# Optimization experiments

Hardware: AMD Instinct MI355X
Metric: run time of the kernel (lower is better)

Reference implementation:

```python
import jax, jax.numpy as jnp
import numpy as np

WINDOW_SIZE = 7
NB_HEADS = 8


def _relative_position_index(ws: int) -> np.ndarray:
    coords = np.stack(np.meshgrid(np.arange(ws), np.arange(ws), indexing='ij'))  # [2, ws, ws]
    flat = coords.reshape(2, -1)  # [2, ws*ws]
    rel = flat[:, :, None] - flat[:, None, :]  # [2, N, N]
    rel = rel.transpose(1, 2, 0)
    rel[:, :, 0] += ws - 1
    rel[:, :, 1] += ws - 1
    rel[:, :, 0] *= 2 * ws - 1
    return rel.sum(-1).astype(np.int64)  # [N, N]


def setup_inputs() -> dict:
    key = jax.random.key(0)
    ks = jax.random.split(key, 7)
    B_, N, C = 2048, WINDOW_SIZE * WINDOW_SIZE, 256
    nW = 64
    return {
        'x': jax.random.normal(ks[0], (B_, N, C), dtype=jnp.float32),
        'mask': jax.random.normal(ks[1], (nW, N, N), dtype=jnp.float32),
        'qkv_w': jax.random.normal(ks[2], (C, 3 * C), dtype=jnp.float32) * 0.02,
        'qkv_b': jax.random.normal(ks[3], (3 * C,), dtype=jnp.float32) * 0.02,
        'proj_w': jax.random.normal(ks[4], (C, C), dtype=jnp.float32) * 0.02,
        'proj_b': jax.random.normal(ks[5], (C,), dtype=jnp.float32) * 0.02,
        'bias_table': jax.random.normal(ks[6], ((2 * WINDOW_SIZE - 1) ** 2, NB_HEADS), dtype=jnp.float32) * 0.02,
    }


def reference(x, mask, qkv_w, qkv_b, proj_w, proj_b, bias_table):
    B_, N, C = x.shape
    h = NB_HEADS
    d = C // h
    rpi = jnp.asarray(_relative_position_index(WINDOW_SIZE))  # [N, N] int

    qkv = x @ qkv_w + qkv_b  # [B_, N, 3C]
    qkv = qkv.reshape(B_, N, 3, h, d).transpose(2, 0, 3, 1, 4)  # [3, B_, h, N, d]
    q, k, v = qkv[0], qkv[1], qkv[2]

    scale = d ** -0.5
    attn = jnp.einsum('bhnd,bhmd->bhnm', q * scale, k)  # [B_, h, N, N]

    # relative position bias gather: [N*N, h] -> [h, N, N]
    bias = bias_table[rpi.reshape(-1)].reshape(N, N, h).transpose(2, 0, 1)
    attn = attn + bias[None]

    nW = mask.shape[0]
    attn = attn.reshape(B_ // nW, nW, h, N, N) + mask[None, :, None]  # broadcast mask over heads
    attn = attn.reshape(B_, h, N, N)
    attn = jax.nn.softmax(attn, axis=-1)

    out = jnp.einsum('bhnm,bhmd->bhnd', attn, v)  # [B_, h, N, d]
    out = out.transpose(0, 2, 1, 3).reshape(B_, N, C)
    return out @ proj_w + proj_b
```

## Files before the change

kernel.cpp:

```cpp
#include <hip/hip_runtime.h>
#include <hip/hip_bf16.h>

typedef __attribute__((ext_vector_type(8))) short bf16x8;
typedef __attribute__((ext_vector_type(4))) float f32x4;

__device__ __forceinline__ void load_lds16(const void* g, void* l) {
    __builtin_amdgcn_global_load_lds(
        (const __attribute__((address_space(1))) unsigned int*)g,
        (__attribute__((address_space(3))) unsigned int*)l, 16, 0, 0);
}

__global__ void k_cvt_x(const float* __restrict__ x, __hip_bfloat16* __restrict__ xb, int n4) {
    for (int i = blockIdx.x * blockDim.x + threadIdx.x; i < n4; i += gridDim.x * blockDim.x) {
        float4 v = ((const float4*)x)[i];
        union { ushort4 u; __hip_bfloat16 h[4]; } o;
        o.h[0] = __float2bfloat16(v.x); o.h[1] = __float2bfloat16(v.y);
        o.h[2] = __float2bfloat16(v.z); o.h[3] = __float2bfloat16(v.w);
        ((ushort4*)xb)[i] = o.u;
    }
}

__global__ void k_prep_w(const float* __restrict__ qkv_w, const float* __restrict__ qkv_b,
                         const float* __restrict__ proj_w, const float* __restrict__ bias_table,
                         __hip_bfloat16* __restrict__ qwT, __hip_bfloat16* __restrict__ pwT,
                         float* __restrict__ qb_s, float* __restrict__ biasH) {
    const float scale = 0.17677669529663687f;
    int i = blockIdx.x * 256 + threadIdx.x;
    if (i < 768 * 256) {
        int nc = i >> 8, kc = i & 255;
        float v = qkv_w[kc * 768 + nc];
        if (nc < 256) v *= scale;
        qwT[i] = __float2bfloat16(v);
    } else if (i < 768 * 256 + 256 * 256) {
        int j = i - 768 * 256;
        int nc = j >> 8, kc = j & 255;
        pwT[j] = __float2bfloat16(proj_w[kc * 256 + nc]);
    } else if (i < 768 * 256 + 256 * 256 + 768) {
        int j = i - (768 * 256 + 256 * 256);
        qb_s[j] = qkv_b[j] * (j < 256 ? scale : 1.f);
    } else if (i < 768 * 256 + 256 * 256 + 768 + 8 * 2401) {
        int j = i - (768 * 256 + 256 * 256 + 768);
        int h = j / 2401, r = j % 2401;
        int n = r / 49, m = r % 49;
        int i1 = n / 7, j1 = n % 7, i2 = m / 7, j2 = m % 7;
        int rpi = (i1 - i2 + 6) * 13 + (j1 - j2 + 6);
        biasH[j] = bias_table[rpi * 8 + h];
    }
}

template <bool OUT_BF16>
__global__ __launch_bounds__(256, 2)
void gemm_bt(const __hip_bfloat16* __restrict__ A,
             const __hip_bfloat16* __restrict__ BT,
             const float* __restrict__ bias,
             void* __restrict__ Cout,
             int M, int N, int K) {
    __shared__ alignas(16) __hip_bfloat16 sA[2][128][64];
    __shared__ alignas(16) __hip_bfloat16 sB[2][128][64];
    const int bn = blockIdx.x, bm = blockIdx.y;
    const int tid = threadIdx.x, wid = tid >> 6, lane = tid & 63;
    const int g = lane >> 4, c0 = lane & 15;
    const int r8 = lane >> 3;
    const int sl = (lane & 7) ^ r8;
    const int wrow = (wid >> 1) * 64, wcol = (wid & 1) * 64;
    const __hip_bfloat16* Abase = A + (size_t)bm * 128 * K;
    const __hip_bfloat16* Bbase = BT + (size_t)bn * 128 * K;
    const int KT = K >> 6;

    f32x4 acc[4][4];
#pragma unroll
    for (int i = 0; i < 4; ++i)
#pragma unroll
        for (int j = 0; j < 4; ++j)
#pragma unroll
            for (int r = 0; r < 4; ++r) acc[i][j][r] = 0.f;

    auto stage = [&](int buf, int kt) {
        const __hip_bfloat16* Ak = Abase + kt * 64;
        const __hip_bfloat16* Bk = Bbase + kt * 64;
        char* la = (char*)&sA[buf][0][0];
        char* lb = (char*)&sB[buf][0][0];
#pragma unroll
        for (int i = 0; i < 4; ++i) {
            int chunk = wid * 4 + i;
            int row = chunk * 8 + r8;
            load_lds16(Ak + (size_t)row * K + sl * 8, la + chunk * 1024);
            load_lds16(Bk + (size_t)row * K + sl * 8, lb + chunk * 1024);
        }
    };

    stage(0, 0);
    __syncthreads();
    for (int kt = 0; kt < KT; ++kt) {
        int cur = kt & 1;
        if (kt + 1 < KT) stage(cur ^ 1, kt + 1);
        const char* la = (const char*)&sA[cur][0][0];
        const char* lb = (const char*)&sB[cur][0][0];
#pragma unroll
        for (int ks = 0; ks < 2; ++ks) {
            bf16x8 af[4], bfr[4];
            int sbyte = ((ks * 4 + g) ^ (c0 & 7)) * 16;
#pragma unroll
            for (int t = 0; t < 4; ++t) {
                int ra = wrow + t * 16 + c0;
                af[t] = *(const bf16x8*)(la + ra * 128 + sbyte);
                int rb = wcol + t * 16 + c0;
                bfr[t] = *(const bf16x8*)(lb + rb * 128 + sbyte);
            }
#pragma unroll
            for (int rt = 0; rt < 4; ++rt)
#pragma unroll
                for (int ct = 0; ct < 4; ++ct)
                    acc[rt][ct] = __builtin_amdgcn_mfma_f32_16x16x32_bf16(
                        af[rt], bfr[ct], acc[rt][ct], 0, 0, 0);
        }
        __syncthreads();
    }

    float bv[4];
#pragma unroll
    for (int ct = 0; ct < 4; ++ct) bv[ct] = bias[bn * 128 + wcol + ct * 16 + c0];
#pragma unroll
    for (int rt = 0; rt < 4; ++rt) {
#pragma unroll
        for (int ct = 0; ct < 4; ++ct) {
#pragma unroll
            for (int reg = 0; reg < 4; ++reg) {
                int row = bm * 128 + wrow + rt * 16 + g * 4 + reg;
                int col = bn * 128 + wcol + ct * 16 + c0;
                float v = acc[rt][ct][reg] + bv[ct];
                if (OUT_BF16)
                    ((__hip_bfloat16*)Cout)[(size_t)row * N + col] = __float2bfloat16(v);
                else
                    ((float*)Cout)[(size_t)row * N + col] = v;
            }
        }
    }
}

__global__ __launch_bounds__(64)
void attn_win(const __hip_bfloat16* __restrict__ qkv,
              const float* __restrict__ mask,
              const float* __restrict__ biasH,
              __hip_bfloat16* __restrict__ attout) {
    __shared__ alignas(16) __hip_bfloat16 vt[32][72];
    __shared__ alignas(16) __hip_bfloat16 pl[64][64];
    const int bh = blockIdx.x;
    const int b = bh >> 3, h = bh & 7;
    const int lane = threadIdx.x & 63, g = lane >> 4, c0 = lane & 15;
    const __hip_bfloat16* qb = qkv + (size_t)b * 49 * 768 + h * 32;

    for (int i = lane; i < 32 * 15; i += 64) {
        int c = i / 15, m = 49 + i % 15;
        vt[c][m] = __float2bfloat16(0.f);
    }
    for (int i = lane; i < 784; i += 64) {
        int m = i >> 4, c2 = (i & 15) * 2;
        ushort2 v = *(const ushort2*)(qb + (size_t)m * 768 + 512 + c2);
        *(unsigned short*)&vt[c2][m] = v.x;
        *(unsigned short*)&vt[c2 + 1][m] = v.y;
    }

    const bf16x8 z8 = {};
    bf16x8 kf[4];
#pragma unroll
    for (int ct = 0; ct < 4; ++ct) {
        int m = ct * 16 + c0;
        kf[ct] = (m < 49) ? *(const bf16x8*)(qb + (size_t)m * 768 + 256 + g * 8) : z8;
    }
    __syncthreads();

    const float* mrow = mask + (size_t)(b & 63) * 2401;
    const float* brow = biasH + (size_t)h * 2401;
    const f32x4 zf = {0.f, 0.f, 0.f, 0.f};

#pragma unroll
    for (int rt = 0; rt < 4; ++rt) {
        int nA = rt * 16 + c0;
        bf16x8 qf = (nA < 49) ? *(const bf16x8*)(qb + (size_t)nA * 768 + g * 8) : z8;
        f32x4 s[4];
#pragma unroll
        for (int ct = 0; ct < 4; ++ct)
            s[ct] = __builtin_amdgcn_mfma_f32_16x16x32_bf16(qf, kf[ct], zf, 0, 0, 0);
#pragma unroll
        for (int reg = 0; reg < 4; ++reg) {
            int n = rt * 16 + 4 * g + reg;
            int nc = n < 49 ? n : 48;
            const float* br = brow + nc * 49;
            const float* mr = mrow + nc * 49;
#pragma unroll
            for (int ct = 0; ct < 4; ++ct) {
                int m = ct * 16 + c0;
                float v = s[ct][reg];
                v = (m < 49) ? v + br[m] + mr[m] : -1e30f;
                s[ct][reg] = v;
            }
            float mx = fmaxf(fmaxf(s[0][reg], s[1][reg]), fmaxf(s[2][reg], s[3][reg]));
            mx = fmaxf(mx, __shfl_xor(mx, 1));
            mx = fmaxf(mx, __shfl_xor(mx, 2));
            mx = fmaxf(mx, __shfl_xor(mx, 4));
            mx = fmaxf(mx, __shfl_xor(mx, 8));
            float sum = 0.f;
#pragma unroll
            for (int ct = 0; ct < 4; ++ct) {
                float e = __expf(s[ct][reg] - mx);
                s[ct][reg] = e;
                sum += e;
            }
            sum += __shfl_xor(sum, 1);
            sum += __shfl_xor(sum, 2);
            sum += __shfl_xor(sum, 4);
            sum += __shfl_xor(sum, 8);
            float inv = 1.f / sum;
#pragma unroll
            for (int ct = 0; ct < 4; ++ct) {
                int m = ct * 16 + c0;
                int byte = (n * 128 + m * 2) ^ ((n & 7) << 4);
                *(__hip_bfloat16*)((char*)&pl[0][0] + byte) = __float2bfloat16(s[ct][reg] * inv);
            }
        }
    }
    __syncthreads();

    f32x4 o[4][2];
#pragma unroll
    for (int rt = 0; rt < 4; ++rt)
#pragma unroll
        for (int ci = 0; ci < 2; ++ci)
#pragma unroll
            for (int r = 0; r < 4; ++r) o[rt][ci][r] = 0.f;
#pragma unroll
    for (int kt = 0; kt < 2; ++kt) {
        bf16x8 pa[4], vb[2];
#pragma unroll
        for (int rt = 0; rt < 4; ++rt) {
            int row = rt * 16 + c0;
            int byte = row * 128 + (((kt * 4 + g) ^ (row & 7)) << 4);
            pa[rt] = *(const bf16x8*)((const char*)&pl[0][0] + byte);
        }
#pragma unroll
        for (int ci = 0; ci < 2; ++ci)
            vb[ci] = *(const bf16x8*)(&vt[ci * 16 + c0][kt * 32 + g * 8]);
#pragma unroll
        for (int rt = 0; rt < 4; ++rt)
#pragma unroll
            for (int ci = 0; ci < 2; ++ci)
                o[rt][ci] = __builtin_amdgcn_mfma_f32_16x16x32_bf16(pa[rt], vb[ci], o[rt][ci], 0, 0, 0);
    }
    __hip_bfloat16* ob = attout + (size_t)b * 49 * 256 + h * 32;
#pragma unroll
    for (int rt = 0; rt < 4; ++rt) {
#pragma unroll
        for (int reg = 0; reg < 4; ++reg) {
            int n = rt * 16 + 4 * g + reg;
            if (n < 49) {
#pragma unroll
                for (int ci = 0; ci < 2; ++ci)
                    ob[(size_t)n * 256 + ci * 16 + c0] = __float2bfloat16(o[rt][ci][reg]);
            }
        }
    }
}

extern "C" void kernel_launch(void* const* d_in, const int* in_sizes, int n_in,
                              void* d_out, int out_size, void* d_ws, size_t ws_size,
                              hipStream_t stream) {
    const float* x          = (const float*)d_in[0];
    const float* mask       = (const float*)d_in[1];
    const float* qkv_w      = (const float*)d_in[2];
    const float* qkv_b      = (const float*)d_in[3];
    const float* proj_w     = (const float*)d_in[4];
    const float* proj_b     = (const float*)d_in[5];
    const float* bias_table = (const float*)d_in[6];

    const int C = 256, N3 = 768, NN = 49;
    const int M  = in_sizes[0] / C;
    const int B_ = M / NN;

    char* ws = (char*)d_ws;
    __hip_bfloat16* qkv_ws = (__hip_bfloat16*)ws;
    size_t off = (size_t)M * N3 * 2;
    __hip_bfloat16* xb  = (__hip_bfloat16*)(ws + off);
    __hip_bfloat16* att = xb;
    off += (size_t)M * C * 2;
    __hip_bfloat16* qwT = (__hip_bfloat16*)(ws + off); off += (size_t)N3 * C * 2;
    __hip_bfloat16* pwT = (__hip_bfloat16*)(ws + off); off += (size_t)C * C * 2;
    float* qb_s  = (float*)(ws + off); off += (size_t)N3 * 4;
    float* biasH = (float*)(ws + off); off += (size_t)8 * 2401 * 4;

    int n4 = (int)((size_t)M * C / 4);
    k_cvt_x<<<2048, 256, 0, stream>>>(x, xb, n4);
    int prep_total = 768 * 256 + 256 * 256 + 768 + 8 * 2401;
    k_prep_w<<<(prep_total + 255) / 256, 256, 0, stream>>>(qkv_w, qkv_b, proj_w, bias_table,
                                                           qwT, pwT, qb_s, biasH);
    gemm_bt<true><<<dim3(N3 / 128, M / 128), 256, 0, stream>>>(xb, qwT, qb_s, qkv_ws, M, N3, C);
    attn_win<<<B_ * 8, 64, 0, stream>>>(qkv_ws, mask, biasH, att);
    gemm_bt<false><<<dim3(C / 128, M / 128), 256, 0, stream>>>(att, pwT, proj_b, d_out, M, C, C);
}
```

Baseline: 402.8 us.

## Precombine bias and mask into MFMA-fragment layout, remap GEMM grid for XCDs

A prep kernel now builds a combined relative-position bias plus window mask tensor per (window, head), stored directly in MFMA accumulator fragment order with padding values baked in. The attention kernel then loads it as coalesced float4 instead of doing scalar gathers and bounds checks. Attention blocks are reordered so blocks sharing a window mask are adjacent, Q fragments and V loads are hoisted and vectorised, the P tile in shared memory is shrunk, and s_setprio is placed around the MFMA sections. Both GEMMs switch to a 1D grid with an XCD-aware block remap to improve L2 locality. In exchange, the prep kernel writes an extra 8MB buffer.

```diff
diff --git a/kernel.cpp b/kernel.cpp
--- a/kernel.cpp
+++ b/kernel.cpp
@@ -20,31 +20,49 @@
     }
 }
 
-__global__ void k_prep_w(const float* __restrict__ qkv_w, const float* __restrict__ qkv_b,
-                         const float* __restrict__ proj_w, const float* __restrict__ bias_table,
-                         __hip_bfloat16* __restrict__ qwT, __hip_bfloat16* __restrict__ pwT,
-                         float* __restrict__ qb_s, float* __restrict__ biasH) {
+__global__ void k_prep(const float* __restrict__ qkv_w, const float* __restrict__ qkv_b,
+                       const float* __restrict__ proj_w, const float* __restrict__ bias_table,
+                       const float* __restrict__ mask,
+                       __hip_bfloat16* __restrict__ qwT, __hip_bfloat16* __restrict__ pwT,
+                       float* __restrict__ qb_s, float* __restrict__ cbt) {
     const float scale = 0.17677669529663687f;
+    const int P1 = 768 * 256, P2 = P1 + 256 * 256, P3 = P2 + 768, P4 = P3 + 64 * 8 * 4 * 4 * 64;
     int i = blockIdx.x * 256 + threadIdx.x;
-    if (i < 768 * 256) {
+    if (i < P1) {
         int nc = i >> 8, kc = i & 255;
         float v = qkv_w[kc * 768 + nc];
         if (nc < 256) v *= scale;
         qwT[i] = __float2bfloat16(v);
-    } else if (i < 768 * 256 + 256 * 256) {
-        int j = i - 768 * 256;
+    } else if (i < P2) {
+        int j = i - P1;
         int nc = j >> 8, kc = j & 255;
         pwT[j] = __float2bfloat16(proj_w[kc * 256 + nc]);
-    } else if (i < 768 * 256 + 256 * 256 + 768) {
-        int j = i - (768 * 256 + 256 * 256);
+    } else if (i < P3) {
+        int j = i - P2;
         qb_s[j] = qkv_b[j] * (j < 256 ? scale : 1.f);
-    } else if (i < 768 * 256 + 256 * 256 + 768 + 8 * 2401) {
-        int j = i - (768 * 256 + 256 * 256 + 768);
-        int h = j / 2401, r = j % 2401;
-        int n = r / 49, m = r % 49;
-        int i1 = n / 7, j1 = n % 7, i2 = m / 7, j2 = m % 7;
-        int rpi = (i1 - i2 + 6) * 13 + (j1 - j2 + 6);
-        biasH[j] = bias_table[rpi * 8 + h];
+    } else if (i < P4) {
+        int j = i - P3;
+        int w = j >> 13;
+        int h = (j >> 10) & 7;
+        int rt = (j >> 8) & 3;
+        int ct = (j >> 6) & 3;
+        int lane = j & 63;
+        int m = ct * 16 + (lane & 15);
+        f32x4 v;
+#pragma unroll
+        for (int reg = 0; reg < 4; ++reg) {
+            int n = rt * 16 + 4 * (lane >> 4) + reg;
+            float val;
+            if (m >= 49) val = -1e30f;
+            else if (n >= 49) val = 0.f;
+            else {
+                int i1 = n / 7, j1 = n % 7, i2 = m / 7, j2 = m % 7;
+                int rpi = (i1 - i2 + 6) * 13 + (j1 - j2 + 6);
+                val = bias_table[rpi * 8 + h] + mask[(w * 49 + n) * 49 + m];
+            }
+            v[reg] = val;
+        }
+        ((f32x4*)cbt)[j] = v;
     }
 }
 
@@ -54,10 +72,15 @@
              const __hip_bfloat16* __restrict__ BT,
              const float* __restrict__ bias,
              void* __restrict__ Cout,
-             int M, int N, int K) {
+             int M, int N, int K, int gridN) {
     __shared__ alignas(16) __hip_bfloat16 sA[2][128][64];
     __shared__ alignas(16) __hip_bfloat16 sB[2][128][64];
-    const int bn = blockIdx.x, bm = blockIdx.y;
+    const int nwg = gridDim.x, bid = blockIdx.x;
+    const int qq = nwg >> 3, rr = nwg & 7;
+    const int xc = bid & 7, oo = bid >> 3;
+    const int wg = (xc < rr ? xc * (qq + 1) : rr * (qq + 1) + (xc - rr) * qq) + oo;
+    const int bm = wg / gridN, bn = wg % gridN;
+
     const int tid = threadIdx.x, wid = tid >> 6, lane = tid & 63;
     const int g = lane >> 4, c0 = lane & 15;
     const int r8 = lane >> 3;
@@ -140,61 +163,66 @@
 
 __global__ __launch_bounds__(64)
 void attn_win(const __hip_bfloat16* __restrict__ qkv,
-              const float* __restrict__ mask,
-              const float* __restrict__ biasH,
+              const float* __restrict__ cbt,
               __hip_bfloat16* __restrict__ attout) {
     __shared__ alignas(16) __hip_bfloat16 vt[32][72];
-    __shared__ alignas(16) __hip_bfloat16 pl[64][64];
-    const int bh = blockIdx.x;
-    const int b = bh >> 3, h = bh & 7;
+    __shared__ alignas(16) __hip_bfloat16 pl[52][64];
+    const int blk = blockIdx.x;
+    const int w = blk >> 8, h = (blk >> 5) & 7, rep = blk & 31;
+    const int b = rep * 64 + w;
     const int lane = threadIdx.x & 63, g = lane >> 4, c0 = lane & 15;
     const __hip_bfloat16* qb = qkv + (size_t)b * 49 * 768 + h * 32;
-
+    const bf16x8 z8 = {};
+
+    bf16x8 kf[4], qf[4];
+#pragma unroll
+    for (int ct = 0; ct < 4; ++ct) {
+        int m = ct * 16 + c0;
+        kf[ct] = (m < 49) ? *(const bf16x8*)(qb + (size_t)m * 768 + 256 + g * 8) : z8;
+    }
+#pragma unroll
+    for (int rt = 0; rt < 4; ++rt) {
+        int n = rt * 16 + c0;
+        qf[rt] = (n < 49) ? *(const bf16x8*)(qb + (size_t)n * 768 + g * 8) : z8;
+    }
+
+#pragma unroll
+    for (int it = 0; it < 4; ++it) {
+        int q = it * 64 + lane;
+        int m = q >> 2, c8 = (q & 3) * 8;
+        if (m < 49) {
+            bf16x8 v8 = *(const bf16x8*)(qb + (size_t)m * 768 + 512 + c8);
+#pragma unroll
+            for (int j = 0; j < 8; ++j)
+                *(short*)&vt[c8 + j][m] = v8[j];
+        }
+    }
     for (int i = lane; i < 32 * 15; i += 64) {
         int c = i / 15, m = 49 + i % 15;
         vt[c][m] = __float2bfloat16(0.f);
     }
-    for (int i = lane; i < 784; i += 64) {
-        int m = i >> 4, c2 = (i & 15) * 2;
-        ushort2 v = *(const ushort2*)(qb + (size_t)m * 768 + 512 + c2);
-        *(unsigned short*)&vt[c2][m] = v.x;
-        *(unsigned short*)&vt[c2 + 1][m] = v.y;
-    }
-
-    const bf16x8 z8 = {};
-    bf16x8 kf[4];
-#pragma unroll
-    for (int ct = 0; ct < 4; ++ct) {
-        int m = ct * 16 + c0;
-        kf[ct] = (m < 49) ? *(const bf16x8*)(qb + (size_t)m * 768 + 256 + g * 8) : z8;
-    }
-    __syncthreads();
-
-    const float* mrow = mask + (size_t)(b & 63) * 2401;
-    const float* brow = biasH + (size_t)h * 2401;
+
+    const f32x4* cbb = (const f32x4*)cbt + ((size_t)(w * 8 + h)) * 1024;
     const f32x4 zf = {0.f, 0.f, 0.f, 0.f};
 
 #pragma unroll
     for (int rt = 0; rt < 4; ++rt) {
-        int nA = rt * 16 + c0;
-        bf16x8 qf = (nA < 49) ? *(const bf16x8*)(qb + (size_t)nA * 768 + g * 8) : z8;
+        f32x4 cb[4];
+#pragma unroll
+        for (int ct = 0; ct < 4; ++ct) cb[ct] = cbb[(rt * 4 + ct) * 64 + lane];
         f32x4 s[4];
+        __builtin_amdgcn_s_setprio(1);
 #pragma unroll
         for (int ct = 0; ct < 4; ++ct)
-            s[ct] = __builtin_amdgcn_mfma_f32_16x16x32_bf16(qf, kf[ct], zf, 0, 0, 0);
+            s[ct] = __builtin_amdgcn_mfma_f32_16x16x32_bf16(qf[rt], kf[ct], zf, 0, 0, 0);
+        __builtin_amdgcn_s_setprio(0);
+#pragma unroll
+        for (int ct = 0; ct < 4; ++ct)
+#pragma unroll
+            for (int reg = 0; reg < 4; ++reg) s[ct][reg] += cb[ct][reg];
 #pragma unroll
         for (int reg = 0; reg < 4; ++reg) {
             int n = rt * 16 + 4 * g + reg;
-            int nc = n < 49 ? n : 48;
-            const float* br = brow + nc * 49;
-            const float* mr = mrow + nc * 49;
-#pragma unroll
-            for (int ct = 0; ct < 4; ++ct) {
-                int m = ct * 16 + c0;
-                float v = s[ct][reg];
-                v = (m < 49) ? v + br[m] + mr[m] : -1e30f;
-                s[ct][reg] = v;
-            }
             float mx = fmaxf(fmaxf(s[0][reg], s[1][reg]), fmaxf(s[2][reg], s[3][reg]));
             mx = fmaxf(mx, __shfl_xor(mx, 1));
             mx = fmaxf(mx, __shfl_xor(mx, 2));
@@ -212,11 +240,13 @@
             sum += __shfl_xor(sum, 4);
             sum += __shfl_xor(sum, 8);
             float inv = 1.f / sum;
-#pragma unroll
-            for (int ct = 0; ct < 4; ++ct) {
-                int m = ct * 16 + c0;
-                int byte = (n * 128 + m * 2) ^ ((n & 7) << 4);
-                *(__hip_bfloat16*)((char*)&pl[0][0] + byte) = __float2bfloat16(s[ct][reg] * inv);
+            if (n < 52) {
+#pragma unroll
+                for (int ct = 0; ct < 4; ++ct) {
+                    int m = ct * 16 + c0;
+                    int byte = (n * 128 + m * 2) ^ ((n & 7) << 4);
+                    *(__hip_bfloat16*)((char*)&pl[0][0] + byte) = __float2bfloat16(s[ct][reg] * inv);
+                }
             }
         }
     }
@@ -235,17 +265,20 @@
 #pragma unroll
         for (int rt = 0; rt < 4; ++rt) {
             int row = rt * 16 + c0;
-            int byte = row * 128 + (((kt * 4 + g) ^ (row & 7)) << 4);
+            int rc = row < 52 ? row : 51;
+            int byte = rc * 128 + (((kt * 4 + g) ^ (rc & 7)) << 4);
             pa[rt] = *(const bf16x8*)((const char*)&pl[0][0] + byte);
         }
 #pragma unroll
         for (int ci = 0; ci < 2; ++ci)
             vb[ci] = *(const bf16x8*)(&vt[ci * 16 + c0][kt * 32 + g * 8]);
+        __builtin_amdgcn_s_setprio(1);
 #pragma unroll
         for (int rt = 0; rt < 4; ++rt)
 #pragma unroll
             for (int ci = 0; ci < 2; ++ci)
                 o[rt][ci] = __builtin_amdgcn_mfma_f32_16x16x32_bf16(pa[rt], vb[ci], o[rt][ci], 0, 0, 0);
+        __builtin_amdgcn_s_setprio(0);
     }
     __hip_bfloat16* ob = attout + (size_t)b * 49 * 256 + h * 32;
 #pragma unroll
@@ -285,15 +318,15 @@
     off += (size_t)M * C * 2;
     __hip_bfloat16* qwT = (__hip_bfloat16*)(ws + off); off += (size_t)N3 * C * 2;
     __hip_bfloat16* pwT = (__hip_bfloat16*)(ws + off); off += (size_t)C * C * 2;
-    float* qb_s  = (float*)(ws + off); off += (size_t)N3 * 4;
-    float* biasH = (float*)(ws + off); off += (size_t)8 * 2401 * 4;
+    float* qb_s = (float*)(ws + off); off += (size_t)N3 * 4;
+    float* cbt  = (float*)(ws + off); off += (size_t)64 * 8 * 4096 * 4;
 
     int n4 = (int)((size_t)M * C / 4);
     k_cvt_x<<<2048, 256, 0, stream>>>(x, xb, n4);
-    int prep_total = 768 * 256 + 256 * 256 + 768 + 8 * 2401;
-    k_prep_w<<<(prep_total + 255) / 256, 256, 0, stream>>>(qkv_w, qkv_b, proj_w, bias_table,
-                                                           qwT, pwT, qb_s, biasH);
-    gemm_bt<true><<<dim3(N3 / 128, M / 128), 256, 0, stream>>>(xb, qwT, qb_s, qkv_ws, M, N3, C);
-    attn_win<<<B_ * 8, 64, 0, stream>>>(qkv_ws, mask, biasH, att);
-    gemm_bt<false><<<dim3(C / 128, M / 128), 256, 0, stream>>>(att, pwT, proj_b, d_out, M, C, C);
-}
+    int prep_total = 768 * 256 + 256 * 256 + 768 + 64 * 8 * 4 * 4 * 64;
+    k_prep<<<(prep_total + 255) / 256, 256, 0, stream>>>(qkv_w, qkv_b, proj_w, bias_table, mask,
+                                                         qwT, pwT, qb_s, cbt);
+    gemm_bt<true><<<(N3 / 128) * (M / 128), 256, 0, stream>>>(xb, qwT, qb_s, qkv_ws, M, N3, C, N3 / 128);
+    attn_win<<<B_ * 8, 64, 0, stream>>>(qkv_ws, cbt, att);
+    gemm_bt<false><<<(C / 128) * (M / 128), 256, 0, stream>>>(att, pwT, proj_b, d_out, M, C, C, C / 128);
+}
```

After: 362.7 us. 1.11x faster.
